# Kernel tuning notes

Measured on AMD Instinct MI355X. Metric: run time of the kernel, lower is better.

The kernel has to match this reference:

```python
import jax, jax.numpy as jnp
import numpy as np

DIM = 192
NH = 6
HD = DIM // NH            # 32
SCALE = HD ** -0.5
HID = int(DIM * 4.0)      # 768
EPS = 1e-5


def _ln(x, g, b):
    m = jnp.mean(x, axis=-1, keepdims=True)
    v = jnp.mean((x - m) ** 2, axis=-1, keepdims=True)
    return (x - m) * jax.lax.rsqrt(v + EPS) * g + b


def setup_inputs() -> dict:
    key = jax.random.key(0)
    ks = jax.random.split(key, 6)
    H = W = T = 48
    B = 1
    L = H * W * T
    return {
        "x": jax.random.normal(ks[0], (B, L, DIM), jnp.float32),
        "norm1_g": jnp.ones((DIM,), jnp.float32),
        "norm1_b": jnp.zeros((DIM,), jnp.float32),
        "qkv_w": jax.random.normal(ks[1], (3 * DIM, DIM), jnp.float32) * 0.02,
        "qkv_b": jnp.zeros((3 * DIM,), jnp.float32),
        "proj_w": jax.random.normal(ks[2], (DIM, DIM), jnp.float32) * 0.02,
        "proj_b": jnp.zeros((DIM,), jnp.float32),
        "norm2_g": jnp.ones((DIM,), jnp.float32),
        "norm2_b": jnp.zeros((DIM,), jnp.float32),
        "fc1_w": jax.random.normal(ks[3], (HID, DIM), jnp.float32) * 0.02,
        "fc1_b": jnp.zeros((HID,), jnp.float32),
        "fc2_w": jax.random.normal(ks[4], (DIM, HID), jnp.float32) * 0.02,
        "fc2_b": jnp.zeros((DIM,), jnp.float32),
        "H": H, "W": W, "T": T,
    }


def reference(x, norm1_g, norm1_b, qkv_w, qkv_b, proj_w, proj_b,
              norm2_g, norm2_b, fc1_w, fc1_b, fc2_w, fc2_b, H, W, T):
    B, L, C = x.shape
    shortcut = x
    h = _ln(x, norm1_g, norm1_b)
    # axial_dims='12' -> extra_dim=3: permute to (B, T, H, W, C), attend over H*W
    h = h.reshape(B, H, W, T, C).transpose(0, 3, 1, 2, 4).reshape(B * T, H * W, C)
    B_, N, _ = h.shape
    qkv = h @ qkv_w.T + qkv_b                                   # (B_, N, 3C)
    # faithful reproduction of the module's unusual reshape mixing batch into head dim
    qkv = qkv.transpose(1, 0, 2).reshape(1, N, 3, NH, B_ * HD).transpose(2, 0, 3, 1, 4)
    q, k, v = qkv[0] * SCALE, qkv[1], qkv[2]                    # (1, NH, N, B_*HD)
    attn = jax.nn.softmax(jnp.einsum('ohnd,ohmd->ohnm', q, k), axis=-1)
    o = jnp.einsum('ohnm,ohmd->ohnd', attn, v)                  # (1, NH, N, B_*HD)
    o = o.transpose(0, 2, 1, 3).reshape(B_, N, C)
    o = o @ proj_w.T + proj_b
    o = o.reshape(B, H * W * T, C)                              # module does NOT undo the permute
    x1 = shortcut + o
    m = _ln(x1, norm2_g, norm2_b)
    m = jax.nn.gelu(m @ fc1_w.T + fc1_b, approximate=False) @ fc2_w.T + fc2_b
    return x1 + m
```

## Files before the change

kernel.cpp:

```cpp
#include <hip/hip_runtime.h>

typedef __bf16 bf16_t;
typedef __attribute__((ext_vector_type(8))) __bf16 bf16x8;
typedef __attribute__((ext_vector_type(4))) float f32x4;

__device__ __forceinline__ float gelu_exact(float x) {
    return 0.5f * x * (1.0f + erff(x * 0.70710678118654752f));
}

#define AS1 __attribute__((address_space(1)))
#define AS3 __attribute__((address_space(3)))

template<int BM, int BN, int EPI>
__global__ __launch_bounds__(256)
void sgemm(const bf16_t* __restrict__ A, int lda,
           const bf16_t* __restrict__ B, int ldb,
           bf16_t* __restrict__ C, int ldc,
           const float* __restrict__ bias,
           float* __restrict__ Cf, const float* __restrict__ resid)
{
    constexpr int MR = BM / 32;
    constexpr int NR = BN / 32;
    __shared__ __align__(16) bf16_t As[BM * 192];
    __shared__ __align__(16) bf16_t Bs[BN * 192];
    const int t = threadIdx.x, w = t >> 6, lane = t & 63;
    const int wr = w >> 1, wc = w & 1;
    const long n0 = (long)blockIdx.x * BN;
    const long m0 = (long)blockIdx.y * BM;

    const int srow = t >> 3;
    const int schx = (t & 7) ^ (srow & 7);
    #pragma unroll
    for (int rc = 0; rc < BM / 32; ++rc)
        #pragma unroll
        for (int kt = 0; kt < 3; ++kt) {
            const bf16_t* src = A + (m0 + rc * 32 + srow) * (long)lda + kt * 64 + schx * 8;
            __builtin_amdgcn_global_load_lds((AS1 void*)(bf16_t*)src,
                (AS3 void*)(As + (rc * 3 + kt) * 2048 + w * 512), 16, 0, 0);
        }
    #pragma unroll
    for (int nc = 0; nc < BN / 32; ++nc)
        #pragma unroll
        for (int kt = 0; kt < 3; ++kt) {
            const bf16_t* src = B + (n0 + nc * 32 + srow) * (long)ldb + kt * 64 + schx * 8;
            __builtin_amdgcn_global_load_lds((AS1 void*)(bf16_t*)src,
                (AS3 void*)(Bs + (nc * 3 + kt) * 2048 + w * 512), 16, 0, 0);
        }
    asm volatile("s_waitcnt vmcnt(0)" ::: "memory");
    __builtin_amdgcn_s_barrier();

    const int lrow = lane & 15, kq4 = lane >> 4;
    f32x4 acc[MR][NR] = {};
    #pragma unroll
    for (int kt = 0; kt < 3; ++kt) {
        bf16x8 af[MR][2], bfr[NR][2];
        #pragma unroll
        for (int i = 0; i < MR; ++i) {
            const int row = wr * (BM / 2) + i * 16 + lrow;
            #pragma unroll
            for (int ks = 0; ks < 2; ++ks) {
                const int sl = (ks * 4 + kq4) ^ (row & 7);
                af[i][ks] = *(const bf16x8*)(As + ((row >> 5) * 3 + kt) * 2048
                                             + (row & 31) * 64 + sl * 8);
            }
        }
        #pragma unroll
        for (int j = 0; j < NR; ++j) {
            const int row = wc * (BN / 2) + j * 16 + lrow;
            #pragma unroll
            for (int ks = 0; ks < 2; ++ks) {
                const int sl = (ks * 4 + kq4) ^ (row & 7);
                bfr[j][ks] = *(const bf16x8*)(Bs + ((row >> 5) * 3 + kt) * 2048
                                              + (row & 31) * 64 + sl * 8);
            }
        }
        #pragma unroll
        for (int ks = 0; ks < 2; ++ks)
            #pragma unroll
            for (int i = 0; i < MR; ++i)
                #pragma unroll
                for (int j = 0; j < NR; ++j)
                    acc[i][j] = __builtin_amdgcn_mfma_f32_16x16x32_bf16(
                        af[i][ks], bfr[j][ks], acc[i][j], 0, 0, 0);
    }

    const int ccol  = lane & 15;
    const int crow4 = (lane >> 4) * 4;
    #pragma unroll
    for (int i = 0; i < MR; ++i) {
        long rowb = m0 + wr * (BM / 2) + i * 16 + crow4;
        #pragma unroll
        for (int j = 0; j < NR; ++j) {
            long col = n0 + wc * (BN / 2) + j * 16 + ccol;
            #pragma unroll
            for (int r = 0; r < 4; ++r) {
                float v = acc[i][j][r];
                long row = rowb + r;
                if constexpr (EPI == 1) {
                    C[row * ldc + col] = (bf16_t)(v + bias[col]);
                } else if constexpr (EPI == 2) {
                    C[row * ldc + col] = (bf16_t)gelu_exact(v + bias[col]);
                } else {
                    long idx = row * ldc + col;
                    Cf[idx] = resid[idx] + v + bias[col];
                }
            }
        }
    }
}

template<int BM, int BN, int EPI, int SWZ>
__global__ __launch_bounds__(256)
void mgemm(const bf16_t* __restrict__ A, int lda, long aBatch,
           const bf16_t* __restrict__ B, int ldb, long bBatch,
           bf16_t* __restrict__ C, int ldc, long cBatch,
           const float* __restrict__ bias, int K,
           float* __restrict__ Cf, const float* __restrict__ resid)
{
    constexpr int MR = BM / 32;
    constexpr int NR = BN / 32;
    constexpr int LPT = BM / 32 + BN / 32;
    __shared__ __align__(16) bf16_t As[2][BM * 64];
    __shared__ __align__(16) bf16_t Bs[2][BN * 64];
    const int t    = threadIdx.x;
    const int w    = t >> 6;
    const int lane = t & 63;
    const int wr   = w >> 1, wc = w & 1;

    unsigned bx = blockIdx.x, by = blockIdx.y, bz = blockIdx.z;
    if constexpr (SWZ) {
        const unsigned gx = gridDim.x, gy = gridDim.y, gz = gridDim.z;
        unsigned lin = (bz * gy + by) * gx + bx;
        const unsigned cpx = (gx * gy * gz) >> 3;
        lin = (lin & 7) * cpx + (lin >> 3);
        bx = lin % gx; lin /= gx;
        by = lin % gy; bz = lin / gy;
    }

    const long n0 = (long)bx * BN;
    const long m0 = (long)by * BM;
    A += (long)bz * aBatch;
    B += (long)bz * bBatch;
    if constexpr (EPI != 3) C += (long)bz * cBatch;

    f32x4 acc[MR][NR] = {};

    const int srow8  = t >> 3;
    const int schunk = (t & 7) ^ (srow8 & 7);
    const int lrow = lane & 15;
    const int kq4  = lane >> 4;

    auto stage = [&](int buf, int k0) {
        #pragma unroll
        for (int c = 0; c < BM / 32; ++c) {
            const bf16_t* src = A + (m0 + c * 32 + srow8) * (long)lda + (k0 + schunk * 8);
            __builtin_amdgcn_global_load_lds(
                (AS1 void*)(bf16_t*)src,
                (AS3 void*)(As[buf] + c * 2048 + w * 512), 16, 0, 0);
        }
        #pragma unroll
        for (int c = 0; c < BN / 32; ++c) {
            const bf16_t* src = B + (n0 + c * 32 + srow8) * (long)ldb + (k0 + schunk * 8);
            __builtin_amdgcn_global_load_lds(
                (AS1 void*)(bf16_t*)src,
                (AS3 void*)(Bs[buf] + c * 2048 + w * 512), 16, 0, 0);
        }
    };

    const int nt = K >> 6;
    stage(0, 0);
    int cur = 0;
    for (int kt = 0; kt < nt; ++kt) {
        if (kt + 1 < nt) {
            stage(cur ^ 1, (kt + 1) << 6);
            if constexpr (LPT == 8)
                asm volatile("s_waitcnt vmcnt(8)" ::: "memory");
            else
                asm volatile("s_waitcnt vmcnt(6)" ::: "memory");
        } else {
            asm volatile("s_waitcnt vmcnt(0)" ::: "memory");
        }
        __builtin_amdgcn_s_barrier();

        bf16x8 af[MR][2], bfr[NR][2];
        #pragma unroll
        for (int i = 0; i < MR; ++i) {
            const int row = wr * (BM / 2) + i * 16 + lrow;
            #pragma unroll
            for (int ks = 0; ks < 2; ++ks) {
                const int ch = (ks * 4 + kq4) ^ (row & 7);
                af[i][ks] = *(const bf16x8*)(As[cur] + row * 64 + ch * 8);
            }
        }
        #pragma unroll
        for (int j = 0; j < NR; ++j) {
            const int row = wc * (BN / 2) + j * 16 + lrow;
            #pragma unroll
            for (int ks = 0; ks < 2; ++ks) {
                const int ch = (ks * 4 + kq4) ^ (row & 7);
                bfr[j][ks] = *(const bf16x8*)(Bs[cur] + row * 64 + ch * 8);
            }
        }
        #pragma unroll
        for (int ks = 0; ks < 2; ++ks)
            #pragma unroll
            for (int i = 0; i < MR; ++i)
                #pragma unroll
                for (int j = 0; j < NR; ++j)
                    acc[i][j] = __builtin_amdgcn_mfma_f32_16x16x32_bf16(
                        af[i][ks], bfr[j][ks], acc[i][j], 0, 0, 0);

        asm volatile("s_waitcnt lgkmcnt(0)" ::: "memory");
        __builtin_amdgcn_s_barrier();
        cur ^= 1;
    }

    const int ccol  = lane & 15;
    const int crow4 = (lane >> 4) * 4;
    #pragma unroll
    for (int i = 0; i < MR; ++i) {
        long rowb = m0 + wr * (BM / 2) + i * 16 + crow4;
        #pragma unroll
        for (int j = 0; j < NR; ++j) {
            long col = n0 + wc * (BN / 2) + j * 16 + ccol;
            #pragma unroll
            for (int r = 0; r < 4; ++r) {
                float v = acc[i][j][r];
                long row = rowb + r;
                if constexpr (EPI == 0) {
                    C[row * ldc + col] = (bf16_t)v;
                } else if constexpr (EPI == 1) {
                    C[row * ldc + col] = (bf16_t)(v + bias[col]);
                } else if constexpr (EPI == 2) {
                    C[row * ldc + col] = (bf16_t)gelu_exact(v + bias[col]);
                } else {
                    long idx = row * ldc + col;
                    Cf[idx] = resid[idx] + v + bias[col];
                }
            }
        }
    }
}

__global__ __launch_bounds__(256)
void transpose_v(const bf16_t* __restrict__ Y, bf16_t* __restrict__ Vt)
{
    __shared__ bf16_t tile[64][80];
    const int h  = blockIdx.z;
    const int e0 = blockIdx.x * 64;
    const int m0 = blockIdx.y * 64;
    const int t  = threadIdx.x;
    const int lr = t >> 3;
    const int lc8 = t & 7;

    #pragma unroll
    for (int i = 0; i < 64; i += 32) {
        int row = lr + i;
        bf16x8 vv = *(const bf16x8*)(Y + (long)(m0 + row) * 27648 + 18432 + h * 1536 + e0 + lc8 * 8);
        int cs = lc8 ^ (row >> 3);
        *(bf16x8*)&tile[row][cs * 8] = vv;
    }
    __syncthreads();
    #pragma unroll
    for (int i = 0; i < 64; i += 32) {
        int er = lr + i;
        bf16x8 vv;
        #pragma unroll
        for (int j = 0; j < 8; ++j) {
            int row = lc8 * 8 + j;
            int cs = (er >> 3) ^ lc8;
            vv[j] = tile[row][cs * 8 + (er & 7)];
        }
        *(bf16x8*)(Vt + ((long)h * 1536 + e0 + er) * 2304 + m0 + lc8 * 8) = vv;
    }
}

__global__ __launch_bounds__(256)
void ln_fast(const float* __restrict__ x, const float* __restrict__ g,
             const float* __restrict__ b, bf16_t* __restrict__ o, int nrows)
{
    const int lane = threadIdx.x & 63;
    const int wave = threadIdx.x >> 6;
    const float g0 = g[lane], g1 = g[lane + 64], g2 = g[lane + 128];
    const float b0 = b[lane], b1 = b[lane + 64], b2 = b[lane + 128];
    for (long row = (long)blockIdx.x * 4 + wave; row < nrows; row += (long)gridDim.x * 4) {
        const float* xr = x + row * 192;
        float v0 = xr[lane], v1 = xr[lane + 64], v2 = xr[lane + 128];
        float s  = v0 + v1 + v2;
        float ss = v0 * v0 + v1 * v1 + v2 * v2;
        #pragma unroll
        for (int d = 32; d > 0; d >>= 1) {
            s  += __shfl_xor(s, d);
            ss += __shfl_xor(ss, d);
        }
        float mean = s * (1.f / 192.f);
        float var  = ss * (1.f / 192.f) - mean * mean;
        float rs   = rsqrtf(var + 1e-5f);
        bf16_t* orow = o + row * 192;
        orow[lane]       = (bf16_t)((v0 - mean) * rs * g0 + b0);
        orow[lane + 64]  = (bf16_t)((v1 - mean) * rs * g1 + b1);
        orow[lane + 128] = (bf16_t)((v2 - mean) * rs * g2 + b2);
    }
}

__global__ __launch_bounds__(256)
void softmax_fast(bf16_t* __restrict__ S)
{
    const float SC = 0.17677669529663687f;
    __shared__ float wmax[4], wsum[4];
    const long base = (long)blockIdx.x * 2304;
    const int t = threadIdx.x;
    const int lane = t & 63, w = t >> 6;
    float v[9];
    float mx = -1e30f;
    #pragma unroll
    for (int i = 0; i < 9; ++i) {
        v[i] = (float)S[base + t + i * 256] * SC;
        mx = fmaxf(mx, v[i]);
    }
    #pragma unroll
    for (int d = 32; d > 0; d >>= 1) mx = fmaxf(mx, __shfl_xor(mx, d));
    if (lane == 0) wmax[w] = mx;
    __syncthreads();
    mx = fmaxf(fmaxf(wmax[0], wmax[1]), fmaxf(wmax[2], wmax[3]));
    float sum = 0.f;
    #pragma unroll
    for (int i = 0; i < 9; ++i) { v[i] = __expf(v[i] - mx); sum += v[i]; }
    #pragma unroll
    for (int d = 32; d > 0; d >>= 1) sum += __shfl_xor(sum, d);
    if (lane == 0) wsum[w] = sum;
    __syncthreads();
    const float inv = 1.f / (wsum[0] + wsum[1] + wsum[2] + wsum[3]);
    #pragma unroll
    for (int i = 0; i < 9; ++i) S[base + t + i * 256] = (bf16_t)(v[i] * inv);
}

__global__ __launch_bounds__(256)
void cast_all(const float* __restrict__ w0, const float* __restrict__ w1,
              const float* __restrict__ w2, const float* __restrict__ w3,
              bf16_t* __restrict__ o0, bf16_t* __restrict__ o1,
              bf16_t* __restrict__ o2, bf16_t* __restrict__ o3)
{
    int i = blockIdx.x * 256 + threadIdx.x;
    if (i < 110592)       o0[i] = (bf16_t)w0[i];
    else if (i < 147456)  o1[i - 110592] = (bf16_t)w1[i - 110592];
    else if (i < 294912)  o2[i - 147456] = (bf16_t)w2[i - 147456];
    else if (i < 442368)  o3[i - 294912] = (bf16_t)w3[i - 294912];
}

extern "C" void kernel_launch(void* const* d_in, const int* in_sizes, int n_in,
                              void* d_out, int out_size, void* d_ws, size_t ws_size,
                              hipStream_t stream)
{
    (void)in_sizes; (void)n_in; (void)out_size; (void)ws_size;
    const float* x      = (const float*)d_in[0];
    const float* n1g    = (const float*)d_in[1];
    const float* n1b    = (const float*)d_in[2];
    const float* qkv_w  = (const float*)d_in[3];
    const float* qkv_b  = (const float*)d_in[4];
    const float* proj_w = (const float*)d_in[5];
    const float* proj_b = (const float*)d_in[6];
    const float* n2g    = (const float*)d_in[7];
    const float* n2b    = (const float*)d_in[8];
    const float* fc1_w  = (const float*)d_in[9];
    const float* fc1_b  = (const float*)d_in[10];
    const float* fc2_w  = (const float*)d_in[11];
    const float* fc2_b  = (const float*)d_in[12];
    float* out = (float*)d_out;

    char* ws = (char*)d_ws;
    size_t off = 0;
    auto alloc = [&](size_t nbytes) -> void* {
        off = (off + 255) & ~(size_t)255;
        void* p = ws + off;
        off += nbytes;
        return p;
    };

    bf16_t* Wq   = (bf16_t*)alloc((size_t)576 * 192 * 2);
    bf16_t* Wp   = (bf16_t*)alloc((size_t)192 * 192 * 2);
    bf16_t* W1   = (bf16_t*)alloc((size_t)768 * 192 * 2);
    bf16_t* W2   = (bf16_t*)alloc((size_t)192 * 768 * 2);
    bf16_t* Hbuf = (bf16_t*)alloc((size_t)110592 * 192 * 2);
    bf16_t* Qkv  = (bf16_t*)alloc((size_t)110592 * 768 * 2);
    bf16_t* Vt   = Qkv + (size_t)110592 * 576;
    bf16_t* Sbuf = (bf16_t*)d_out;

    cast_all<<<1728, 256, 0, stream>>>(qkv_w, proj_w, fc1_w, fc2_w, Wq, Wp, W1, W2);

    ln_fast<<<2048, 256, 0, stream>>>(x, n1g, n1b, Hbuf, 110592);
    sgemm<96, 64, 1><<<dim3(9, 1152, 1), 256, 0, stream>>>(
        Hbuf, 192, Wq, 192, Qkv, 576, qkv_b, nullptr, nullptr);
    transpose_v<<<dim3(24, 36, 6), 256, 0, stream>>>(Qkv, Vt);
    mgemm<128, 128, 0, 1><<<dim3(18, 18, 6), 256, 0, stream>>>(
        Qkv, 27648, 1536, Qkv + 9216, 27648, 1536,
        Sbuf, 2304, (long)2304 * 2304, nullptr, 1536, nullptr, nullptr);
    softmax_fast<<<13824, 256, 0, stream>>>(Sbuf);
    mgemm<128, 128, 0, 1><<<dim3(12, 18, 6), 256, 0, stream>>>(
        Sbuf, 2304, (long)2304 * 2304, Vt, 2304, (long)1536 * 2304,
        Hbuf, 9216, 1536, nullptr, 2304, nullptr, nullptr);
    sgemm<96, 64, 3><<<dim3(3, 1152, 1), 256, 0, stream>>>(
        Hbuf, 192, Wp, 192, nullptr, 192, proj_b, out, x);
    ln_fast<<<2048, 256, 0, stream>>>(out, n2g, n2b, Hbuf, 110592);
    sgemm<96, 64, 2><<<dim3(12, 1152, 1), 256, 0, stream>>>(
        Hbuf, 192, W1, 192, Qkv, 768, fc1_b, nullptr, nullptr);
    mgemm<128, 64, 3, 0><<<dim3(3, 864, 1), 256, 0, stream>>>(
        Qkv, 768, 0, W2, 768, 0, nullptr, 192, 0, fc2_b, 768, out, out);
}
```

Before: 802.4 us.

## Fuse projection GEMM with residual and LayerNorm2; route other GEMMs through mgemm

Adds a proj_ln kernel that computes the projection GEMM with double-buffered K staging. It applies bias and residual, writes the fp32 output, and then computes LayerNorm2 from an LDS copy of the 64-row tile to emit the bf16 input for fc1. This removes the separate LayerNorm launch and its re-read of the fp32 activation. The QKV and fc1 GEMMs now use the pipelined mgemm with 128-row tiles instead of the single-shot sgemm, which is deleted. The fused kernel uses 64KB of LDS per block, which may limit occupancy, and its LayerNorm reduction is done by only four threads per row.

```diff
diff --git a/kernel.cpp b/kernel.cpp
--- a/kernel.cpp
+++ b/kernel.cpp
@@ -10,104 +10,6 @@
 
 #define AS1 __attribute__((address_space(1)))
 #define AS3 __attribute__((address_space(3)))
-
-template<int BM, int BN, int EPI>
-__global__ __launch_bounds__(256)
-void sgemm(const bf16_t* __restrict__ A, int lda,
-           const bf16_t* __restrict__ B, int ldb,
-           bf16_t* __restrict__ C, int ldc,
-           const float* __restrict__ bias,
-           float* __restrict__ Cf, const float* __restrict__ resid)
-{
-    constexpr int MR = BM / 32;
-    constexpr int NR = BN / 32;
-    __shared__ __align__(16) bf16_t As[BM * 192];
-    __shared__ __align__(16) bf16_t Bs[BN * 192];
-    const int t = threadIdx.x, w = t >> 6, lane = t & 63;
-    const int wr = w >> 1, wc = w & 1;
-    const long n0 = (long)blockIdx.x * BN;
-    const long m0 = (long)blockIdx.y * BM;
-
-    const int srow = t >> 3;
-    const int schx = (t & 7) ^ (srow & 7);
-    #pragma unroll
-    for (int rc = 0; rc < BM / 32; ++rc)
-        #pragma unroll
-        for (int kt = 0; kt < 3; ++kt) {
-            const bf16_t* src = A + (m0 + rc * 32 + srow) * (long)lda + kt * 64 + schx * 8;
-            __builtin_amdgcn_global_load_lds((AS1 void*)(bf16_t*)src,
-                (AS3 void*)(As + (rc * 3 + kt) * 2048 + w * 512), 16, 0, 0);
-        }
-    #pragma unroll
-    for (int nc = 0; nc < BN / 32; ++nc)
-        #pragma unroll
-        for (int kt = 0; kt < 3; ++kt) {
-            const bf16_t* src = B + (n0 + nc * 32 + srow) * (long)ldb + kt * 64 + schx * 8;
-            __builtin_amdgcn_global_load_lds((AS1 void*)(bf16_t*)src,
-                (AS3 void*)(Bs + (nc * 3 + kt) * 2048 + w * 512), 16, 0, 0);
-        }
-    asm volatile("s_waitcnt vmcnt(0)" ::: "memory");
-    __builtin_amdgcn_s_barrier();
-
-    const int lrow = lane & 15, kq4 = lane >> 4;
-    f32x4 acc[MR][NR] = {};
-    #pragma unroll
-    for (int kt = 0; kt < 3; ++kt) {
-        bf16x8 af[MR][2], bfr[NR][2];
-        #pragma unroll
-        for (int i = 0; i < MR; ++i) {
-            const int row = wr * (BM / 2) + i * 16 + lrow;
-            #pragma unroll
-            for (int ks = 0; ks < 2; ++ks) {
-                const int sl = (ks * 4 + kq4) ^ (row & 7);
-                af[i][ks] = *(const bf16x8*)(As + ((row >> 5) * 3 + kt) * 2048
-                                             + (row & 31) * 64 + sl * 8);
-            }
-        }
-        #pragma unroll
-        for (int j = 0; j < NR; ++j) {
-            const int row = wc * (BN / 2) + j * 16 + lrow;
-            #pragma unroll
-            for (int ks = 0; ks < 2; ++ks) {
-                const int sl = (ks * 4 + kq4) ^ (row & 7);
-                bfr[j][ks] = *(const bf16x8*)(Bs + ((row >> 5) * 3 + kt) * 2048
-                                              + (row & 31) * 64 + sl * 8);
-            }
-        }
-        #pragma unroll
-        for (int ks = 0; ks < 2; ++ks)
-            #pragma unroll
-            for (int i = 0; i < MR; ++i)
-                #pragma unroll
-                for (int j = 0; j < NR; ++j)
-                    acc[i][j] = __builtin_amdgcn_mfma_f32_16x16x32_bf16(
-                        af[i][ks], bfr[j][ks], acc[i][j], 0, 0, 0);
-    }
-
-    const int ccol  = lane & 15;
-    const int crow4 = (lane >> 4) * 4;
-    #pragma unroll
-    for (int i = 0; i < MR; ++i) {
-        long rowb = m0 + wr * (BM / 2) + i * 16 + crow4;
-        #pragma unroll
-        for (int j = 0; j < NR; ++j) {
-            long col = n0 + wc * (BN / 2) + j * 16 + ccol;
-            #pragma unroll
-            for (int r = 0; r < 4; ++r) {
-                float v = acc[i][j][r];
-                long row = rowb + r;
-                if constexpr (EPI == 1) {
-                    C[row * ldc + col] = (bf16_t)(v + bias[col]);
-                } else if constexpr (EPI == 2) {
-                    C[row * ldc + col] = (bf16_t)gelu_exact(v + bias[col]);
-                } else {
-                    long idx = row * ldc + col;
-                    Cf[idx] = resid[idx] + v + bias[col];
-                }
-            }
-        }
-    }
-}
 
 template<int BM, int BN, int EPI, int SWZ>
 __global__ __launch_bounds__(256)
@@ -239,6 +141,126 @@
                 }
             }
         }
+    }
+}
+
+__global__ __launch_bounds__(256)
+void proj_ln(const bf16_t* __restrict__ A,
+             const bf16_t* __restrict__ B,
+             const float* __restrict__ bias,
+             const float* __restrict__ resid,
+             float* __restrict__ out,
+             const float* __restrict__ g, const float* __restrict__ bb,
+             bf16_t* __restrict__ H)
+{
+    constexpr int MR = 2, NR = 6;
+    __shared__ __align__(16) char smem[65536];
+    bf16_t* As = (bf16_t*)smem;
+    bf16_t* Bs = (bf16_t*)(smem + 16384);
+    float*  Xs = (float*)smem;
+    const int t = threadIdx.x, w = t >> 6, lane = t & 63;
+    const int wr = w >> 1, wc = w & 1;
+    const long m0 = (long)blockIdx.x * 64;
+
+    const int srow8  = t >> 3;
+    const int schunk = (t & 7) ^ (srow8 & 7);
+    const int lrow = lane & 15, kq4 = lane >> 4;
+
+    auto stage = [&](int buf, int k0) {
+        #pragma unroll
+        for (int c = 0; c < 2; ++c) {
+            const bf16_t* src = A + (m0 + c * 32 + srow8) * 192L + (k0 + schunk * 8);
+            __builtin_amdgcn_global_load_lds((AS1 void*)(bf16_t*)src,
+                (AS3 void*)(As + buf * 4096 + c * 2048 + w * 512), 16, 0, 0);
+        }
+        #pragma unroll
+        for (int c = 0; c < 6; ++c) {
+            const bf16_t* src = B + (c * 32 + srow8) * 192L + (k0 + schunk * 8);
+            __builtin_amdgcn_global_load_lds((AS1 void*)(bf16_t*)src,
+                (AS3 void*)(Bs + buf * 12288 + c * 2048 + w * 512), 16, 0, 0);
+        }
+    };
+
+    f32x4 acc[MR][NR] = {};
+    stage(0, 0);
+    int cur = 0;
+    for (int kt = 0; kt < 3; ++kt) {
+        if (kt < 2) {
+            stage(cur ^ 1, (kt + 1) * 64);
+            asm volatile("s_waitcnt vmcnt(8)" ::: "memory");
+        } else {
+            asm volatile("s_waitcnt vmcnt(0)" ::: "memory");
+        }
+        __builtin_amdgcn_s_barrier();
+
+        bf16x8 af[MR][2], bfr[NR][2];
+        #pragma unroll
+        for (int i = 0; i < MR; ++i) {
+            const int row = wr * 32 + i * 16 + lrow;
+            #pragma unroll
+            for (int ks = 0; ks < 2; ++ks) {
+                const int ch = (ks * 4 + kq4) ^ (row & 7);
+                af[i][ks] = *(const bf16x8*)(As + cur * 4096 + row * 64 + ch * 8);
+            }
+        }
+        #pragma unroll
+        for (int j = 0; j < NR; ++j) {
+            const int row = wc * 96 + j * 16 + lrow;
+            #pragma unroll
+            for (int ks = 0; ks < 2; ++ks) {
+                const int ch = (ks * 4 + kq4) ^ (row & 7);
+                bfr[j][ks] = *(const bf16x8*)(Bs + cur * 12288 + row * 64 + ch * 8);
+            }
+        }
+        #pragma unroll
+        for (int ks = 0; ks < 2; ++ks)
+            #pragma unroll
+            for (int i = 0; i < MR; ++i)
+                #pragma unroll
+                for (int j = 0; j < NR; ++j)
+                    acc[i][j] = __builtin_amdgcn_mfma_f32_16x16x32_bf16(
+                        af[i][ks], bfr[j][ks], acc[i][j], 0, 0, 0);
+
+        asm volatile("s_waitcnt lgkmcnt(0)" ::: "memory");
+        __builtin_amdgcn_s_barrier();
+        cur ^= 1;
+    }
+
+    const int ccol = lane & 15, crow4 = (lane >> 4) * 4;
+    #pragma unroll
+    for (int i = 0; i < MR; ++i) {
+        const int rl = wr * 32 + i * 16 + crow4;
+        #pragma unroll
+        for (int j = 0; j < NR; ++j) {
+            const int col = wc * 96 + j * 16 + ccol;
+            #pragma unroll
+            for (int r = 0; r < 4; ++r) {
+                long idx = (m0 + rl + r) * 192L + col;
+                float v = resid[idx] + acc[i][j][r] + bias[col];
+                out[idx] = v;
+                Xs[(rl + r) * 196 + col] = v;
+            }
+        }
+    }
+    __syncthreads();
+
+    {
+        const int row = t >> 2, q = t & 3;
+        const float* xr = Xs + row * 196 + q * 48;
+        float s = 0.f, ss = 0.f;
+        #pragma unroll
+        for (int c = 0; c < 48; ++c) { float v = xr[c]; s += v; ss += v * v; }
+        s += __shfl_xor(s, 1); ss += __shfl_xor(ss, 1);
+        s += __shfl_xor(s, 2); ss += __shfl_xor(ss, 2);
+        const float mean = s * (1.f / 192.f);
+        const float var  = ss * (1.f / 192.f) - mean * mean;
+        const float rs   = rsqrtf(var + 1e-5f);
+        bf16_t* hr = H + (m0 + row) * 192 + q * 48;
+        const float* gq = g + q * 48;
+        const float* bq = bb + q * 48;
+        #pragma unroll
+        for (int c = 0; c < 48; ++c)
+            hr[c] = (bf16_t)((xr[c] - mean) * rs * gq[c] + bq[c]);
     }
 }
 
@@ -389,8 +411,8 @@
     cast_all<<<1728, 256, 0, stream>>>(qkv_w, proj_w, fc1_w, fc2_w, Wq, Wp, W1, W2);
 
     ln_fast<<<2048, 256, 0, stream>>>(x, n1g, n1b, Hbuf, 110592);
-    sgemm<96, 64, 1><<<dim3(9, 1152, 1), 256, 0, stream>>>(
-        Hbuf, 192, Wq, 192, Qkv, 576, qkv_b, nullptr, nullptr);
+    mgemm<128, 64, 1, 0><<<dim3(9, 864, 1), 256, 0, stream>>>(
+        Hbuf, 192, 0, Wq, 192, 0, Qkv, 576, 0, qkv_b, 192, nullptr, nullptr);
     transpose_v<<<dim3(24, 36, 6), 256, 0, stream>>>(Qkv, Vt);
     mgemm<128, 128, 0, 1><<<dim3(18, 18, 6), 256, 0, stream>>>(
         Qkv, 27648, 1536, Qkv + 9216, 27648, 1536,
@@ -399,11 +421,10 @@
     mgemm<128, 128, 0, 1><<<dim3(12, 18, 6), 256, 0, stream>>>(
         Sbuf, 2304, (long)2304 * 2304, Vt, 2304, (long)1536 * 2304,
         Hbuf, 9216, 1536, nullptr, 2304, nullptr, nullptr);
-    sgemm<96, 64, 3><<<dim3(3, 1152, 1), 256, 0, stream>>>(
-        Hbuf, 192, Wp, 192, nullptr, 192, proj_b, out, x);
-    ln_fast<<<2048, 256, 0, stream>>>(out, n2g, n2b, Hbuf, 110592);
-    sgemm<96, 64, 2><<<dim3(12, 1152, 1), 256, 0, stream>>>(
-        Hbuf, 192, W1, 192, Qkv, 768, fc1_b, nullptr, nullptr);
+    proj_ln<<<1728, 256, 0, stream>>>(
+        Hbuf, Wp, proj_b, x, out, n2g, n2b, Hbuf);
+    mgemm<128, 128, 2, 0><<<dim3(6, 864, 1), 256, 0, stream>>>(
+        Hbuf, 192, 0, W1, 192, 0, Qkv, 768, 0, fc1_b, 192, nullptr, nullptr);
     mgemm<128, 64, 3, 0><<<dim3(3, 864, 1), 256, 0, stream>>>(
         Qkv, 768, 0, W2, 768, 0, nullptr, 192, 0, fc2_b, 768, out, out);
 }
```

Result: faster. 785.9 us (-2.1%).
